# Kernel tuning notes

Hardware: AMD Instinct MI355X
Metric: run time of the kernel (lower is better)

## Reference

```python
import jax, jax.numpy as jnp
import numpy as np

B, S, H, U = 32, 2048, 1024, 1024


def setup_inputs() -> dict:
    key = jax.random.key(0)
    ks = jax.random.split(key, 5)
    sc = 1.0 / np.sqrt(H)
    return {
        "hidden_t": jax.random.normal(ks[0], (B, H), jnp.float32),
        "hiddens": jax.random.normal(ks[1], (B, S, H), jnp.float32),
        "W1": jax.random.normal(ks[2], (H, U), jnp.float32) * sc,
        "b1": jnp.zeros((U,), jnp.float32),
        "W2": jax.random.normal(ks[3], (H, U), jnp.float32) * sc,
        "b2": jnp.zeros((U,), jnp.float32),
        "V": jax.random.normal(ks[4], (U, 1), jnp.float32) * sc,
        "bV": jnp.zeros((1,), jnp.float32),
    }


def reference(hidden_t, hiddens, W1, b1, W2, b2, V, bV):
    # proj of encoder states: [B,S,U]; proj of decoder state broadcast over time: [B,1,U]
    keys = jnp.einsum("bsh,hu->bsu", hiddens, W1) + b1
    query = (hidden_t @ W2 + b2)[:, None, :]
    score = jnp.tanh(keys + query) @ V + bV            # [B,S,1]
    attention_weights = jax.nn.softmax(score, axis=1)  # softmax over seq axis
    context_vector = jnp.sum(attention_weights * hiddens, axis=1)  # [B,H]
    return context_vector, attention_weights
```

## Files before the change

kernel.cpp:

```cpp
#include <hip/hip_runtime.h>
#include <hip/hip_bf16.h>
#include <cstdint>

#define S_LEN 2048
#define B_SZ  32
#define H_DIM 1024
#define U_DIM 1024

using short8  = __attribute__((ext_vector_type(8))) short;
using floatx4 = __attribute__((ext_vector_type(4))) float;

typedef __attribute__((address_space(3))) void lds_void;
typedef const __attribute__((address_space(1))) void glb_void;
#define GLD16(g, s) __builtin_amdgcn_global_load_lds((glb_void*)(g), (lds_void*)(s), 16, 0, 0)

__device__ __forceinline__ unsigned short f32_to_bf16_rne(float f) {
    unsigned int u = __float_as_uint(f);
    unsigned int r = (u + 0x7fffu + ((u >> 16) & 1u)) >> 16;
    return (unsigned short)r;
}

__global__ __launch_bounds__(256)
void cast_hiddens_kernel(const float* __restrict__ src, unsigned short* __restrict__ dst) {
    const size_t i = ((size_t)blockIdx.x * 256 + threadIdx.x) * 8;
    float4 a = *(const float4*)(src + i);
    float4 b = *(const float4*)(src + i + 4);
    ushort4 lo, hi;
    lo.x = f32_to_bf16_rne(a.x); lo.y = f32_to_bf16_rne(a.y);
    lo.z = f32_to_bf16_rne(a.z); lo.w = f32_to_bf16_rne(a.w);
    hi.x = f32_to_bf16_rne(b.x); hi.y = f32_to_bf16_rne(b.y);
    hi.z = f32_to_bf16_rne(b.z); hi.w = f32_to_bf16_rne(b.w);
    *(ushort4*)(dst + i)     = lo;
    *(ushort4*)(dst + i + 4) = hi;
}

__global__ void transpose_cast_w1(const float* __restrict__ W1,
                                  unsigned short* __restrict__ W1t) {
    __shared__ float tile[32][33];
    const int tx = threadIdx.x, ty = threadIdx.y;
    const int u0 = blockIdx.x * 32, h0 = blockIdx.y * 32;
#pragma unroll
    for (int i = 0; i < 4; ++i)
        tile[ty * 4 + i][tx] = W1[(size_t)(h0 + ty * 4 + i) * U_DIM + u0 + tx];
    __syncthreads();
#pragma unroll
    for (int i = 0; i < 4; ++i)
        W1t[(size_t)(u0 + ty * 4 + i) * H_DIM + h0 + tx] =
            f32_to_bf16_rne(tile[tx][ty * 4 + i]);
}

__global__ __launch_bounds__(128)
void query_kernel_v2(const float* __restrict__ hidden_t,
                     const float* __restrict__ W2,
                     const float* __restrict__ b1,
                     const float* __restrict__ b2,
                     float* __restrict__ query) {
    const int b  = blockIdx.z;
    const int hc = blockIdx.y;
    const int u  = blockIdx.x * 128 + threadIdx.x;
    const float* ht = hidden_t + b * H_DIM + hc * 128;
    const float* w  = W2 + (size_t)hc * 128 * U_DIM + u;
    float acc = (hc == 0) ? (b1[u] + b2[u]) : 0.f;
#pragma unroll 8
    for (int h = 0; h < 128; ++h)
        acc = fmaf(ht[h], w[(size_t)h * U_DIM], acc);
    atomicAdd(&query[b * U_DIM + u], acc);
}

__global__ __launch_bounds__(512)
void keys_score_v5(const unsigned short* __restrict__ hb,
                   const unsigned short* __restrict__ W1t,
                   const float* __restrict__ query,
                   const float* __restrict__ V,
                   float* __restrict__ scores) {
    __shared__ unsigned short As[2][256 * 64];
    __shared__ unsigned short Bs[2][256 * 64];

    const int tid = threadIdx.x;
    const int w = tid >> 6, l = tid & 63;
    const int q = l >> 4, r = l & 15, r7 = l & 7;
    const int wr = w >> 2, wc = w & 3;

    const int bid = blockIdx.x;
    const int wg  = (bid & 7) * 128 + (bid >> 3);
    const int m0 = (wg >> 2) << 8;
    const int n0 = (wg & 3) << 8;

    const int srow = l >> 3;
    const int gch  = ((l & 7) ^ srow) << 3;

    const unsigned short* gA = hb  + ((size_t)(m0 + w * 8 + srow) << 10) + gch;
    const unsigned short* gB = W1t + ((size_t)(n0 + w * 8 + srow) << 10) + gch;
    const int wbase = (w * 8) << 6;

    floatx4 acc[8][4];
#pragma unroll
    for (int mt = 0; mt < 8; ++mt)
#pragma unroll
        for (int nt = 0; nt < 4; ++nt)
            acc[mt][nt] = (floatx4){0.f, 0.f, 0.f, 0.f};

#define STAGE_A(t, d)                                                         \
    {                                                                         \
        const unsigned short* _g = gA + ((size_t)(t) << 6);                   \
        _Pragma("unroll")                                                     \
        for (int _i = 0; _i < 4; ++_i)                                        \
            GLD16(_g + ((size_t)(_i * 64) << 10), &As[d][wbase + _i * 4096]); \
    }
#define STAGE_B(t, d)                                                         \
    {                                                                         \
        const unsigned short* _g = gB + ((size_t)(t) << 6);                   \
        _Pragma("unroll")                                                     \
        for (int _i = 0; _i < 4; ++_i)                                        \
            GLD16(_g + ((size_t)(_i * 64) << 10), &Bs[d][wbase + _i * 4096]); \
    }

    const int arow0 = (wr * 128 + r) << 6;
    const int brow0 = (wc * 64 + r) << 6;
    const int ch0 = (q ^ r7) << 3;
    const int ch1 = ((4 | q) ^ r7) << 3;

    STAGE_A(0, 0); STAGE_B(0, 0); STAGE_A(1, 1);
    asm volatile("s_waitcnt vmcnt(4)" ::: "memory");
    __builtin_amdgcn_s_barrier();

    for (int kt = 0; kt < 16; ++kt) {
        const int c = kt & 1, nc = c ^ 1;
        const int tB = (kt + 1 < 16) ? kt + 1 : 15;
        const int tA = (kt + 2 < 16) ? kt + 2 : 15;
        short8 af[8], b0, b1;

#pragma unroll
        for (int mt = 0; mt < 8; ++mt)
            af[mt] = *(const short8*)&As[c][arow0 + mt * 1024 + ch0];
        b0 = *(const short8*)&Bs[c][brow0 + ch0];
        b1 = *(const short8*)&Bs[c][brow0 + 1024 + ch0];
        STAGE_B(tB, nc);
        __builtin_amdgcn_s_barrier();
        asm volatile("s_waitcnt lgkmcnt(0)" ::: "memory");
        __builtin_amdgcn_s_setprio(1);
#pragma unroll
        for (int mt = 0; mt < 8; ++mt) {
            acc[mt][0] = __builtin_amdgcn_mfma_f32_16x16x32_bf16(af[mt], b0, acc[mt][0], 0, 0, 0);
            acc[mt][1] = __builtin_amdgcn_mfma_f32_16x16x32_bf16(af[mt], b1, acc[mt][1], 0, 0, 0);
        }
        __builtin_amdgcn_s_setprio(0);
        __builtin_amdgcn_s_barrier();

        b0 = *(const short8*)&Bs[c][brow0 + 2048 + ch0];
        b1 = *(const short8*)&Bs[c][brow0 + 3072 + ch0];
        __builtin_amdgcn_s_barrier();
        asm volatile("s_waitcnt lgkmcnt(0)" ::: "memory");
        __builtin_amdgcn_s_setprio(1);
#pragma unroll
        for (int mt = 0; mt < 8; ++mt) {
            acc[mt][2] = __builtin_amdgcn_mfma_f32_16x16x32_bf16(af[mt], b0, acc[mt][2], 0, 0, 0);
            acc[mt][3] = __builtin_amdgcn_mfma_f32_16x16x32_bf16(af[mt], b1, acc[mt][3], 0, 0, 0);
        }
        __builtin_amdgcn_s_setprio(0);
        __builtin_amdgcn_s_barrier();

#pragma unroll
        for (int mt = 0; mt < 8; ++mt)
            af[mt] = *(const short8*)&As[c][arow0 + mt * 1024 + ch1];
        b0 = *(const short8*)&Bs[c][brow0 + ch1];
        b1 = *(const short8*)&Bs[c][brow0 + 1024 + ch1];
        __builtin_amdgcn_s_barrier();
        asm volatile("s_waitcnt lgkmcnt(0)" ::: "memory");
        __builtin_amdgcn_s_setprio(1);
#pragma unroll
        for (int mt = 0; mt < 8; ++mt) {
            acc[mt][0] = __builtin_amdgcn_mfma_f32_16x16x32_bf16(af[mt], b0, acc[mt][0], 0, 0, 0);
            acc[mt][1] = __builtin_amdgcn_mfma_f32_16x16x32_bf16(af[mt], b1, acc[mt][1], 0, 0, 0);
        }
        __builtin_amdgcn_s_setprio(0);
        __builtin_amdgcn_s_barrier();

        b0 = *(const short8*)&Bs[c][brow0 + 2048 + ch1];
        b1 = *(const short8*)&Bs[c][brow0 + 3072 + ch1];
        STAGE_A(tA, c);
        asm volatile("s_waitcnt vmcnt(4)" ::: "memory");
        __builtin_amdgcn_s_barrier();
        asm volatile("s_waitcnt lgkmcnt(0)" ::: "memory");
        __builtin_amdgcn_s_setprio(1);
#pragma unroll
        for (int mt = 0; mt < 8; ++mt) {
            acc[mt][2] = __builtin_amdgcn_mfma_f32_16x16x32_bf16(af[mt], b0, acc[mt][2], 0, 0, 0);
            acc[mt][3] = __builtin_amdgcn_mfma_f32_16x16x32_bf16(af[mt], b1, acc[mt][3], 0, 0, 0);
        }
        __builtin_amdgcn_s_setprio(0);
        __builtin_amdgcn_s_barrier();
    }
#undef STAGE_A
#undef STAGE_B

    const float* qrow = query + (m0 >> 11) * U_DIM;
#pragma unroll
    for (int mt = 0; mt < 8; ++mt) {
#pragma unroll
        for (int reg = 0; reg < 4; ++reg) {
            float sum = 0.f;
#pragma unroll
            for (int nt = 0; nt < 4; ++nt) {
                const int cc = n0 + wc * 64 + nt * 16 + r;
                float x = acc[mt][nt][reg] + qrow[cc];
                x = fminf(fmaxf(x, -15.f), 15.f);
                float e = __expf(2.f * x);
                float t = (e - 1.f) / (e + 1.f);
                sum = fmaf(t, V[cc], sum);
            }
            sum += __shfl_xor(sum, 1);
            sum += __shfl_xor(sum, 2);
            sum += __shfl_xor(sum, 4);
            sum += __shfl_xor(sum, 8);
            if (r == 0)
                atomicAdd(&scores[m0 + wr * 128 + mt * 16 + q * 4 + reg], sum);
        }
    }
}

__global__ __launch_bounds__(256)
void keys_score_v1(const float* __restrict__ hiddens,
                   const unsigned short* __restrict__ W1t,
                   const float* __restrict__ query,
                   const float* __restrict__ V,
                   float* __restrict__ scores) {
    __shared__ unsigned short As[128][40];
    __shared__ unsigned short Bs[128][40];
    const int tid = threadIdx.x;
    const int lane = tid & 63, wave = tid >> 6;
    const int q = lane >> 4, r = lane & 15;
    const int wr = wave >> 1, wc = wave & 1;
    const int m0 = blockIdx.y * 128, n0 = blockIdx.x * 128;
    const int arow = tid >> 3, achunk = tid & 7;
    const int brow = tid >> 2, bchunk = tid & 3;
    floatx4 acc[4][4];
#pragma unroll
    for (int mt = 0; mt < 4; ++mt)
#pragma unroll
        for (int nt = 0; nt < 4; ++nt)
            acc[mt][nt] = (floatx4){0.f, 0.f, 0.f, 0.f};
    for (int kt = 0; kt < H_DIM / 32; ++kt) {
        const float* ag = hiddens + (size_t)(m0 + arow) * H_DIM + kt * 32 + achunk * 4;
#pragma unroll
        for (int i = 0; i < 4; ++i) {
            float4 f = *(const float4*)(ag + (size_t)i * 32 * H_DIM);
            ushort4 h;
            h.x = f32_to_bf16_rne(f.x); h.y = f32_to_bf16_rne(f.y);
            h.z = f32_to_bf16_rne(f.z); h.w = f32_to_bf16_rne(f.w);
            *(ushort4*)&As[arow + i * 32][achunk * 4] = h;
        }
        const unsigned short* bg = W1t + (size_t)(n0 + brow) * H_DIM + kt * 32 + bchunk * 8;
#pragma unroll
        for (int i = 0; i < 2; ++i)
            *(uint4*)&Bs[brow + i * 64][bchunk * 8] = *(const uint4*)(bg + (size_t)i * 64 * H_DIM);
        __syncthreads();
        short8 af[4], bfr[4];
#pragma unroll
        for (int mt = 0; mt < 4; ++mt)
            af[mt] = *(const short8*)&As[wr * 64 + mt * 16 + r][q * 8];
#pragma unroll
        for (int nt = 0; nt < 4; ++nt)
            bfr[nt] = *(const short8*)&Bs[wc * 64 + nt * 16 + r][q * 8];
#pragma unroll
        for (int mt = 0; mt < 4; ++mt)
#pragma unroll
            for (int nt = 0; nt < 4; ++nt)
                acc[mt][nt] = __builtin_amdgcn_mfma_f32_16x16x32_bf16(
                    af[mt], bfr[nt], acc[mt][nt], 0, 0, 0);
        __syncthreads();
    }
    const float* qrow = query + (m0 >> 11) * U_DIM;
#pragma unroll
    for (int mt = 0; mt < 4; ++mt) {
#pragma unroll
        for (int reg = 0; reg < 4; ++reg) {
            float sum = 0.f;
#pragma unroll
            for (int nt = 0; nt < 4; ++nt) {
                const int cc = n0 + wc * 64 + nt * 16 + r;
                float x = acc[mt][nt][reg] + qrow[cc];
                x = fminf(fmaxf(x, -15.f), 15.f);
                float e = __expf(2.f * x);
                float t = (e - 1.f) / (e + 1.f);
                sum = fmaf(t, V[cc], sum);
            }
            sum += __shfl_xor(sum, 1);
            sum += __shfl_xor(sum, 2);
            sum += __shfl_xor(sum, 4);
            sum += __shfl_xor(sum, 8);
            if (r == 0)
                atomicAdd(&scores[m0 + wr * 64 + mt * 16 + q * 4 + reg], sum);
        }
    }
}

__global__ __launch_bounds__(256)
void softmax_stats_kernel(const float* __restrict__ scores,
                          float2* __restrict__ stats) {
    const int b = blockIdx.x, tid = threadIdx.x;
    const int wave = tid >> 6, lane = tid & 63;
    const float* src = scores + b * S_LEN;
    float v[8];
    float m = -1e30f;
#pragma unroll
    for (int i = 0; i < 8; ++i) { v[i] = src[tid + i * 256]; m = fmaxf(m, v[i]); }
#pragma unroll
    for (int off = 32; off >= 1; off >>= 1) m = fmaxf(m, __shfl_xor(m, off));
    __shared__ float red[4];
    if (lane == 0) red[wave] = m;
    __syncthreads();
    m = fmaxf(fmaxf(red[0], red[1]), fmaxf(red[2], red[3]));
    __syncthreads();
    float s = 0.f;
#pragma unroll
    for (int i = 0; i < 8; ++i) s += __expf(v[i] - m);
#pragma unroll
    for (int off = 32; off >= 1; off >>= 1) s += __shfl_xor(s, off);
    if (lane == 0) red[wave] = s;
    __syncthreads();
    if (tid == 0) {
        s = red[0] + red[1] + red[2] + red[3];
        stats[b] = make_float2(m, 1.f / s);
    }
}

__global__ __launch_bounds__(256)
void context_partial_kernel(const float* __restrict__ scores,
                            const float2* __restrict__ stats,
                            const float* __restrict__ hiddens,
                            float* __restrict__ out_w,
                            float* __restrict__ partial) {
    const int b = blockIdx.y, sc = blockIdx.x;
    const int tid = threadIdx.x;
    __shared__ float wsm[128];

    const float2 st = stats[b];
    if (tid < 128) {
        const int s = sc * 128 + tid;
        const float w = __expf(scores[b * S_LEN + s] - st.x) * st.y;
        wsm[tid] = w;
        out_w[b * S_LEN + s] = w;
    }
    __syncthreads();

    const float* hbase = hiddens + ((size_t)b * S_LEN + sc * 128) * H_DIM + tid * 4;
    float4 acc = make_float4(0.f, 0.f, 0.f, 0.f);
#pragma unroll 4
    for (int s = 0; s < 128; ++s) {
        const float w = wsm[s];
        float4 hv = *(const float4*)(hbase + (size_t)s * H_DIM);
        acc.x = fmaf(w, hv.x, acc.x);
        acc.y = fmaf(w, hv.y, acc.y);
        acc.z = fmaf(w, hv.z, acc.z);
        acc.w = fmaf(w, hv.w, acc.w);
    }
    *(float4*)(partial + ((size_t)(b * 16 + sc) << 10) + tid * 4) = acc;
}

__global__ __launch_bounds__(256)
void context_reduce_kernel(const float* __restrict__ partial,
                           float* __restrict__ out_ctx) {
    const int b = blockIdx.x, tid = threadIdx.x;
    float4 acc = make_float4(0.f, 0.f, 0.f, 0.f);
#pragma unroll
    for (int sc = 0; sc < 16; ++sc) {
        float4 p = *(const float4*)(partial + ((size_t)(b * 16 + sc) << 10) + tid * 4);
        acc.x += p.x; acc.y += p.y; acc.z += p.z; acc.w += p.w;
    }
    *(float4*)(out_ctx + b * H_DIM + tid * 4) = acc;
}

extern "C" void kernel_launch(void* const* d_in, const int* in_sizes, int n_in,
                              void* d_out, int out_size, void* d_ws, size_t ws_size,
                              hipStream_t stream) {
    const float* hidden_t = (const float*)d_in[0];
    const float* hiddens  = (const float*)d_in[1];
    const float* W1       = (const float*)d_in[2];
    const float* b1       = (const float*)d_in[3];
    const float* W2       = (const float*)d_in[4];
    const float* b2       = (const float*)d_in[5];
    const float* V        = (const float*)d_in[6];

    float* out_ctx = (float*)d_out;
    float* out_w   = (float*)d_out + B_SZ * H_DIM;

    char* ws = (char*)d_ws;
    unsigned short* W1t = (unsigned short*)ws;
    float*  query   = (float*)(ws + (2u << 20));
    float*  scores  = query + B_SZ * U_DIM;
    float2* stats   = (float2*)(scores + B_SZ * S_LEN);
    float*  partial = (float*)(ws + (3u << 20));
    unsigned short* hb = (unsigned short*)(ws + (6u << 20));
    const size_t need = (6u << 20) + (size_t)B_SZ * S_LEN * H_DIM * 2;

    hipMemsetAsync(query,  0, (size_t)B_SZ * U_DIM * sizeof(float), stream);
    hipMemsetAsync(scores, 0, (size_t)B_SZ * S_LEN * sizeof(float), stream);

    transpose_cast_w1<<<dim3(32, 32), dim3(32, 8), 0, stream>>>(W1, W1t);
    query_kernel_v2<<<dim3(8, 8, B_SZ), 128, 0, stream>>>(hidden_t, W2, b1, b2, query);

    if (ws_size >= need) {
        cast_hiddens_kernel<<<32768, 256, 0, stream>>>(hiddens, hb);
        keys_score_v5<<<(B_SZ * S_LEN / 256) * (U_DIM / 256), 512, 0, stream>>>(
            hb, W1t, query, V, scores);
    } else {
        keys_score_v1<<<dim3(U_DIM / 128, (B_SZ * S_LEN) / 128), 256, 0, stream>>>(
            hiddens, W1t, query, V, scores);
    }

    softmax_stats_kernel<<<B_SZ, 256, 0, stream>>>(scores, stats);
    context_partial_kernel<<<dim3(16, B_SZ), 256, 0, stream>>>(
        scores, stats, hiddens, out_w, partial);
    context_reduce_kernel<<<B_SZ, 256, 0, stream>>>(partial, out_ctx);
}
```

Measured before the change: 635.6 us.

## Software-pipeline LDS fragment loads across MFMA phases and use rcp-based tanh

Restructures the GEMM main loop so each phase's A/B fragments are loaded from LDS while the previous phase's MFMAs run. It uses two fragment register sets, partial lgkmcnt waits and sched_barriers, and prefetches the next k-tile's first fragments at the end of each iteration. It also requests two workgroups per CU via launch bounds. The tanh epilogue drops the clamp and uses a reciprocal-based formula. The cost is higher register pressure, which could cause spills given the launch-bound constraint. The tanh relies on expf saturating safely for large inputs.

```diff
diff --git a/kernel.cpp b/kernel.cpp
--- a/kernel.cpp
+++ b/kernel.cpp
@@ -18,6 +18,11 @@
     unsigned int u = __float_as_uint(f);
     unsigned int r = (u + 0x7fffu + ((u >> 16) & 1u)) >> 16;
     return (unsigned short)r;
+}
+
+__device__ __forceinline__ float fast_tanh(float x) {
+    float e = __expf(2.f * x);
+    return 1.f - 2.f * __builtin_amdgcn_rcpf(e + 1.f);
 }
 
 __global__ __launch_bounds__(256)
@@ -67,8 +72,8 @@
     atomicAdd(&query[b * U_DIM + u], acc);
 }
 
-__global__ __launch_bounds__(512)
-void keys_score_v5(const unsigned short* __restrict__ hb,
+__global__ __launch_bounds__(512, 2)
+void keys_score_v6(const unsigned short* __restrict__ hb,
                    const unsigned short* __restrict__ W1t,
                    const float* __restrict__ query,
                    const float* __restrict__ V,
@@ -123,70 +128,82 @@
     STAGE_A(0, 0); STAGE_B(0, 0); STAGE_A(1, 1);
     asm volatile("s_waitcnt vmcnt(4)" ::: "memory");
     __builtin_amdgcn_s_barrier();
+    __builtin_amdgcn_sched_barrier(0);
+
+    short8 af0[8], af1[8], b00, b01, b02, b03, b10, b11, b12, b13;
+#pragma unroll
+    for (int mt = 0; mt < 8; ++mt)
+        af0[mt] = *(const short8*)&As[0][arow0 + mt * 1024 + ch0];
+    b00 = *(const short8*)&Bs[0][brow0 + ch0];
+    b01 = *(const short8*)&Bs[0][brow0 + 1024 + ch0];
 
     for (int kt = 0; kt < 16; ++kt) {
         const int c = kt & 1, nc = c ^ 1;
         const int tB = (kt + 1 < 16) ? kt + 1 : 15;
         const int tA = (kt + 2 < 16) ? kt + 2 : 15;
-        short8 af[8], b0, b1;
+
+        b02 = *(const short8*)&Bs[c][brow0 + 2048 + ch0];
+        b03 = *(const short8*)&Bs[c][brow0 + 3072 + ch0];
+        STAGE_B(tB, nc);
+        __builtin_amdgcn_s_barrier();
+        asm volatile("s_waitcnt lgkmcnt(2)" ::: "memory");
+        __builtin_amdgcn_sched_barrier(0);
+        __builtin_amdgcn_s_setprio(1);
+#pragma unroll
+        for (int mt = 0; mt < 8; ++mt) {
+            acc[mt][0] = __builtin_amdgcn_mfma_f32_16x16x32_bf16(af0[mt], b00, acc[mt][0], 0, 0, 0);
+            acc[mt][1] = __builtin_amdgcn_mfma_f32_16x16x32_bf16(af0[mt], b01, acc[mt][1], 0, 0, 0);
+        }
+        __builtin_amdgcn_s_setprio(0);
+        __builtin_amdgcn_s_barrier();
 
 #pragma unroll
         for (int mt = 0; mt < 8; ++mt)
-            af[mt] = *(const short8*)&As[c][arow0 + mt * 1024 + ch0];
-        b0 = *(const short8*)&Bs[c][brow0 + ch0];
-        b1 = *(const short8*)&Bs[c][brow0 + 1024 + ch0];
-        STAGE_B(tB, nc);
-        __builtin_amdgcn_s_barrier();
-        asm volatile("s_waitcnt lgkmcnt(0)" ::: "memory");
+            af1[mt] = *(const short8*)&As[c][arow0 + mt * 1024 + ch1];
+        b10 = *(const short8*)&Bs[c][brow0 + ch1];
+        b11 = *(const short8*)&Bs[c][brow0 + 1024 + ch1];
+        __builtin_amdgcn_s_barrier();
+        asm volatile("s_waitcnt lgkmcnt(10)" ::: "memory");
+        __builtin_amdgcn_sched_barrier(0);
         __builtin_amdgcn_s_setprio(1);
 #pragma unroll
         for (int mt = 0; mt < 8; ++mt) {
-            acc[mt][0] = __builtin_amdgcn_mfma_f32_16x16x32_bf16(af[mt], b0, acc[mt][0], 0, 0, 0);
-            acc[mt][1] = __builtin_amdgcn_mfma_f32_16x16x32_bf16(af[mt], b1, acc[mt][1], 0, 0, 0);
+            acc[mt][2] = __builtin_amdgcn_mfma_f32_16x16x32_bf16(af0[mt], b02, acc[mt][2], 0, 0, 0);
+            acc[mt][3] = __builtin_amdgcn_mfma_f32_16x16x32_bf16(af0[mt], b03, acc[mt][3], 0, 0, 0);
         }
         __builtin_amdgcn_s_setprio(0);
         __builtin_amdgcn_s_barrier();
 
-        b0 = *(const short8*)&Bs[c][brow0 + 2048 + ch0];
-        b1 = *(const short8*)&Bs[c][brow0 + 3072 + ch0];
-        __builtin_amdgcn_s_barrier();
-        asm volatile("s_waitcnt lgkmcnt(0)" ::: "memory");
+        b12 = *(const short8*)&Bs[c][brow0 + 2048 + ch1];
+        b13 = *(const short8*)&Bs[c][brow0 + 3072 + ch1];
+        __builtin_amdgcn_s_barrier();
+        asm volatile("s_waitcnt lgkmcnt(2)" ::: "memory");
+        __builtin_amdgcn_sched_barrier(0);
         __builtin_amdgcn_s_setprio(1);
 #pragma unroll
         for (int mt = 0; mt < 8; ++mt) {
-            acc[mt][2] = __builtin_amdgcn_mfma_f32_16x16x32_bf16(af[mt], b0, acc[mt][2], 0, 0, 0);
-            acc[mt][3] = __builtin_amdgcn_mfma_f32_16x16x32_bf16(af[mt], b1, acc[mt][3], 0, 0, 0);
+            acc[mt][0] = __builtin_amdgcn_mfma_f32_16x16x32_bf16(af1[mt], b10, acc[mt][0], 0, 0, 0);
+            acc[mt][1] = __builtin_amdgcn_mfma_f32_16x16x32_bf16(af1[mt], b11, acc[mt][1], 0, 0, 0);
         }
         __builtin_amdgcn_s_setprio(0);
         __builtin_amdgcn_s_barrier();
 
-#pragma unroll
-        for (int mt = 0; mt < 8; ++mt)
-            af[mt] = *(const short8*)&As[c][arow0 + mt * 1024 + ch1];
-        b0 = *(const short8*)&Bs[c][brow0 + ch1];
-        b1 = *(const short8*)&Bs[c][brow0 + 1024 + ch1];
-        __builtin_amdgcn_s_barrier();
-        asm volatile("s_waitcnt lgkmcnt(0)" ::: "memory");
-        __builtin_amdgcn_s_setprio(1);
-#pragma unroll
-        for (int mt = 0; mt < 8; ++mt) {
-            acc[mt][0] = __builtin_amdgcn_mfma_f32_16x16x32_bf16(af[mt], b0, acc[mt][0], 0, 0, 0);
-            acc[mt][1] = __builtin_amdgcn_mfma_f32_16x16x32_bf16(af[mt], b1, acc[mt][1], 0, 0, 0);
-        }
-        __builtin_amdgcn_s_setprio(0);
-        __builtin_amdgcn_s_barrier();
-
-        b0 = *(const short8*)&Bs[c][brow0 + 2048 + ch1];
-        b1 = *(const short8*)&Bs[c][brow0 + 3072 + ch1];
         STAGE_A(tA, c);
         asm volatile("s_waitcnt vmcnt(4)" ::: "memory");
         __builtin_amdgcn_s_barrier();
-        asm volatile("s_waitcnt lgkmcnt(0)" ::: "memory");
+        __builtin_amdgcn_sched_barrier(0);
+#pragma unroll
+        for (int mt = 0; mt < 8; ++mt)
+            af0[mt] = *(const short8*)&As[nc][arow0 + mt * 1024 + ch0];
+        b00 = *(const short8*)&Bs[nc][brow0 + ch0];
+        b01 = *(const short8*)&Bs[nc][brow0 + 1024 + ch0];
+        asm volatile("s_waitcnt lgkmcnt(10)" ::: "memory");
+        __builtin_amdgcn_sched_barrier(0);
         __builtin_amdgcn_s_setprio(1);
 #pragma unroll
         for (int mt = 0; mt < 8; ++mt) {
-            acc[mt][2] = __builtin_amdgcn_mfma_f32_16x16x32_bf16(af[mt], b0, acc[mt][2], 0, 0, 0);
-            acc[mt][3] = __builtin_amdgcn_mfma_f32_16x16x32_bf16(af[mt], b1, acc[mt][3], 0, 0, 0);
+            acc[mt][2] = __builtin_amdgcn_mfma_f32_16x16x32_bf16(af1[mt], b12, acc[mt][2], 0, 0, 0);
+            acc[mt][3] = __builtin_amdgcn_mfma_f32_16x16x32_bf16(af1[mt], b13, acc[mt][3], 0, 0, 0);
         }
         __builtin_amdgcn_s_setprio(0);
         __builtin_amdgcn_s_barrier();
@@ -203,10 +220,7 @@
 #pragma unroll
             for (int nt = 0; nt < 4; ++nt) {
                 const int cc = n0 + wc * 64 + nt * 16 + r;
-                float x = acc[mt][nt][reg] + qrow[cc];
-                x = fminf(fmaxf(x, -15.f), 15.f);
-                float e = __expf(2.f * x);
-                float t = (e - 1.f) / (e + 1.f);
+                float t = fast_tanh(acc[mt][nt][reg] + qrow[cc]);
                 sum = fmaf(t, V[cc], sum);
             }
             sum += __shfl_xor(sum, 1);
@@ -279,10 +293,7 @@
 #pragma unroll
             for (int nt = 0; nt < 4; ++nt) {
                 const int cc = n0 + wc * 64 + nt * 16 + r;
-                float x = acc[mt][nt][reg] + qrow[cc];
-                x = fminf(fmaxf(x, -15.f), 15.f);
-                float e = __expf(2.f * x);
-                float t = (e - 1.f) / (e + 1.f);
+                float t = fast_tanh(acc[mt][nt][reg] + qrow[cc]);
                 sum = fmaf(t, V[cc], sum);
             }
             sum += __shfl_xor(sum, 1);
@@ -402,7 +413,7 @@
 
     if (ws_size >= need) {
         cast_hiddens_kernel<<<32768, 256, 0, stream>>>(hiddens, hb);
-        keys_score_v5<<<(B_SZ * S_LEN / 256) * (U_DIM / 256), 512, 0, stream>>>(
+        keys_score_v6<<<(B_SZ * S_LEN / 256) * (U_DIM / 256), 512, 0, stream>>>(
             hb, W1t, query, V, scores);
     } else {
         keys_score_v1<<<dim3(U_DIM / 128, (B_SZ * S_LEN) / 128), 256, 0, stream>>>(
```

New measurement: 640.6 us. About the same (+0.8%).
